# Performance work log

Hardware: AMD Instinct MI355X
Metric: run time of the kernel (lower is better)

Reference implementation:

```python
import jax, jax.numpy as jnp
import numpy as np

EPS = 1e-7  # K.epsilon()


def setup_inputs() -> dict:
    key = jax.random.key(0)
    k1, k2, k3, k4, k5, k6 = jax.random.split(key, 6)
    B, S, D = 128, 1024, 256
    ATT, QDIM = 128, 128
    inp = {
        "key": jax.random.normal(k1, (B, S, D), dtype=jnp.float32),
        "query": jax.random.normal(k2, (QDIM, 1), dtype=jnp.float32),
        "mask": jax.random.randint(k3, (B, S), 0, 2, dtype=jnp.int32),
        # learned params (keras 'normal' init ~ N(0, 0.05))
        "W": 0.05 * jax.random.normal(k4, (D, ATT), dtype=jnp.float32),
        "b": 0.05 * jax.random.normal(k5, (ATT,), dtype=jnp.float32),
        "W_u": 0.05 * jax.random.normal(k6, (ATT, QDIM), dtype=jnp.float32),
    }
    return inp


def reference(key, query, mask, W, b, W_u):
    # uit = tanh(key @ W + b): (B,S,ATT)
    uit = jnp.tanh(jnp.einsum("bsd,da->bsa", key, W) + b)
    # u = W_u @ query: (ATT,1)
    u = W_u @ query
    # scores: (B,S)
    ait = jnp.einsum("bsa,a->bs", uit, u[:, 0])
    ait = jnp.exp(ait)
    ait = ait * mask.astype(jnp.float32)
    ait = ait / (jnp.sum(ait, axis=1, keepdims=True) + EPS)
    # weighted sum over sequence -> (B,D); value == key
    out = jnp.einsum("bs,bsd->bd", ait, key)
    return out
```

## Files before the change

### kernel.cpp

```cpp
#include <hip/hip_runtime.h>
#include <hip/hip_bf16.h>
#include <math.h>

#define EPS_F 1e-7f

constexpr int Bn = 128, Sn = 1024, Dn = 256, ATTn = 128, QDn = 128;
constexpr int Mn = Bn * Sn;
constexpr int BM = 128;
constexpr int NBLK = Mn / BM;
constexpr int NJ = ATTn / 16;

typedef short short8 __attribute__((ext_vector_type(8)));
typedef float f32x4  __attribute__((ext_vector_type(4)));

__device__ inline void split_bf(float f, ushort& hi, ushort& lo) {
    uint fb = __float_as_uint(f);
    hi = (ushort)(fb >> 16);
    float hf = __uint_as_float(fb & 0xffff0000u);
    float lf = f - hf;
    __hip_bfloat16 lb = __float2bfloat16(lf);
    __builtin_memcpy(&lo, &lb, 2);
}

__device__ inline float tanh_fast(float x) {
    float cx = fminf(9.0f, fmaxf(-9.0f, x));
    float e = __builtin_amdgcn_exp2f(cx * 2.8853900817779268f);
    return (e - 1.0f) * __builtin_amdgcn_rcpf(e + 1.0f);
}

__device__ inline void gload_lds16(const void* g, void* lds_base) {
    __builtin_amdgcn_global_load_lds(
        (const __attribute__((address_space(1))) unsigned int*)g,
        (__attribute__((address_space(3))) unsigned int*)lds_base, 16, 0, 0);
}

#define MFMA_BF16 __builtin_amdgcn_mfma_f32_16x16x32_bf16


__global__ __launch_bounds__(256) void k_prep(
    const float* __restrict__ Wu, const float* __restrict__ q,
    float* __restrict__ u,
    const float* __restrict__ W,
    ushort* __restrict__ Bhi, ushort* __restrict__ Blo)
{
    if (blockIdx.x == 0) {
        __shared__ float qs[QDn];
        int t = threadIdx.x;
        if (t < QDn) qs[t] = q[t];
        __syncthreads();
        if (t < ATTn) {
            float acc = 0.f;
            #pragma unroll 8
            for (int j = 0; j < QDn; ++j) acc += Wu[t * QDn + j] * qs[j];
            u[t] = acc;
        }
        return;
    }
    int gid  = (blockIdx.x - 1) * 256 + threadIdx.x;
    int lane = gid & 63;
    int j    = (gid >> 6) & 7;
    int ks   = gid >> 9;
    int col  = j * 16 + (lane & 15);
    int kb   = ks * 32 + (lane >> 4) * 8;
    #pragma unroll
    for (int i = 0; i < 8; ++i) {
        float f = W[(size_t)(kb + i) * ATTn + col];
        ushort h, l;
        split_bf(f, h, l);
        size_t idx = (size_t)gid * 8 + i;
        Bhi[idx] = h; Blo[idx] = l;
    }
}

__device__ __forceinline__ void stage_quarter(
    float4* dst, const ushort* __restrict__ Bhi,
    const ushort* __restrict__ Blo, int q, int t, int w)
{
    #pragma unroll
    for (int i = 0; i < 4; ++i) {
        int c   = i * 512 + t;
        int ks2 = c >> 10;
        int hp  = (c >> 9) & 1;
        int idx = c & 511;
        const ushort* src = (hp ? Blo : Bhi)
                          + ((size_t)((q * 2 + ks2) * 512 + idx)) * 8;
        gload_lds16(src, dst + (i * 512 + w * 64));
    }
}

template<int KS>
__device__ __forceinline__ void kstep(
    float4* smem, const float* kb,
    float4 (&kv)[4][2], f32x4 (&acc)[NJ], int lane)
{
    const float4* buf = smem + ((KS >> 1) & 1) * 2048;
    constexpr int S  = KS & 3;
    constexpr int S2 = KS & 1;
    short8 ah, al;
    {
        float4 v0 = kv[S][0], v1 = kv[S][1];
        float f[8] = {v0.x, v0.y, v0.z, v0.w, v1.x, v1.y, v1.z, v1.w};
        #pragma unroll
        for (int i = 0; i < 8; ++i) {
            ushort h, l;
            split_bf(f[i], h, l);
            ah[i] = (short)h; al[i] = (short)l;
        }
    }
    if (KS + 4 < 8) {
        kv[S][0] = *(const float4*)(kb + (KS + 4) * 32);
        kv[S][1] = *(const float4*)(kb + (KS + 4) * 32 + 4);
    }
    const float4* Bh = buf + S2 * 1024 + lane;
    const float4* Bl = Bh + 512;
    short8 bh[3], bl[3];
    bh[0] = *(const short8*)(Bh);
    bl[0] = *(const short8*)(Bl);
    bh[1] = *(const short8*)(Bh + 64);
    bl[1] = *(const short8*)(Bl + 64);
    bh[2] = *(const short8*)(Bh + 128);
    bl[2] = *(const short8*)(Bl + 128);
    #pragma unroll
    for (int j = 0; j < NJ; ++j) {
        const int slot = j % 3;
        short8 cbh = bh[slot], cbl = bl[slot];
        if (j + 3 < NJ) {
            bh[slot] = *(const short8*)(Bh + (j + 3) * 64);
            bl[slot] = *(const short8*)(Bl + (j + 3) * 64);
        }
        acc[j] = MFMA_BF16(ah, cbh, acc[j], 0, 0, 0);
        acc[j] = MFMA_BF16(ah, cbl, acc[j], 0, 0, 0);
        acc[j] = MFMA_BF16(al, cbh, acc[j], 0, 0, 0);
    }
}

__global__ __launch_bounds__(512)
__attribute__((amdgpu_waves_per_eu(4, 4))) void k_scores(
    const float*  __restrict__ key,
    const ushort* __restrict__ Bhi, const ushort* __restrict__ Blo,
    const float*  __restrict__ bias, const float* __restrict__ u,
    const int*    __restrict__ mask,
    float* __restrict__ P, float* __restrict__ den)
{
    __shared__ float4 smem[4096];
    float*  esp   = (float*)smem;
    float4* partp = smem + 64;

    const int t    = threadIdx.x;
    const int lane = t & 63;
    const int w    = t >> 6;
    const int gb   = blockIdx.x;
    const int row0 = gb * BM;
    const int l15  = lane & 15;
    const int lg   = lane >> 4;

    const float* kb = key + (size_t)(row0 + w * 16 + l15) * Dn + lg * 8;

    f32x4 acc[NJ];
    #pragma unroll
    for (int j = 0; j < NJ; ++j) acc[j] = (f32x4){0.f, 0.f, 0.f, 0.f};

    float4 kv[4][2];
    #pragma unroll
    for (int s = 0; s < 4; ++s) {
        kv[s][0] = *(const float4*)(kb + s * 32);
        kv[s][1] = *(const float4*)(kb + s * 32 + 4);
    }

    stage_quarter(smem, Bhi, Blo, 0, t, w);
    __syncthreads();

    stage_quarter(smem + 2048, Bhi, Blo, 1, t, w);
    kstep<0>(smem, kb, kv, acc, lane);
    kstep<1>(smem, kb, kv, acc, lane);
    __syncthreads();

    stage_quarter(smem, Bhi, Blo, 2, t, w);
    kstep<2>(smem, kb, kv, acc, lane);
    kstep<3>(smem, kb, kv, acc, lane);
    __syncthreads();

    stage_quarter(smem + 2048, Bhi, Blo, 3, t, w);
    kstep<4>(smem, kb, kv, acc, lane);
    kstep<5>(smem, kb, kv, acc, lane);
    __syncthreads();

    kstep<6>(smem, kb, kv, acc, lane);
    kstep<7>(smem, kb, kv, acc, lane);
    __syncthreads();

    float s4[4] = {0.f, 0.f, 0.f, 0.f};
    #pragma unroll
    for (int j = 0; j < NJ; ++j) {
        int col = j * 16 + l15;
        float bv = bias[col], uvv = u[col];
        #pragma unroll
        for (int reg = 0; reg < 4; ++reg)
            s4[reg] += tanh_fast(acc[j][reg] + bv) * uvv;
    }
    #pragma unroll
    for (int reg = 0; reg < 4; ++reg) {
        float s = s4[reg];
        s += __shfl_xor(s, 1);
        s += __shfl_xor(s, 2);
        s += __shfl_xor(s, 4);
        s += __shfl_xor(s, 8);
        if (l15 == 0) {
            int rl = w * 16 + lg * 4 + reg;
            esp[rl] = __builtin_amdgcn_exp2f(s * 1.4426950408889634f)
                      * (float)mask[row0 + rl];
        }
    }
    __syncthreads();

    if (t < 64) {
        float v = esp[t] + esp[t + 64];
        #pragma unroll
        for (int m = 1; m < 64; m <<= 1) v += __shfl_xor(v, m);
        if (t == 0) den[gb] = v;
    }

    {
        const float4* kt = (const float4*)(key + (size_t)(row0 + w * 16) * Dn);
        float4 a2 = make_float4(0.f, 0.f, 0.f, 0.f);
        #pragma unroll 4
        for (int s2 = 0; s2 < 16; ++s2) {
            float wv   = esp[w * 16 + s2];
            float4 kvv = kt[(size_t)s2 * 64 + lane];
            a2.x += wv * kvv.x; a2.y += wv * kvv.y;
            a2.z += wv * kvv.z; a2.w += wv * kvv.w;
        }
        partp[w * 64 + lane] = a2;
    }
    __syncthreads();

    if (t < 64) {
        float4 o = partp[t];
        #pragma unroll
        for (int wv = 1; wv < 8; ++wv) {
            float4 p = partp[wv * 64 + t];
            o.x += p.x; o.y += p.y; o.z += p.z; o.w += p.w;
        }
        *(float4*)(P + (size_t)gb * Dn + t * 4) = o;
    }
}

__global__ __launch_bounds__(256) void k_final(const float* __restrict__ P,
        const float* __restrict__ den, float* __restrict__ out) {
    int b = blockIdx.x, t = threadIdx.x;
    float dtot = 0.f;
    #pragma unroll
    for (int k = 0; k < 8; ++k) dtot += den[b * 8 + k];
    float o = 0.f;
    #pragma unroll
    for (int k = 0; k < 8; ++k) o += P[(size_t)(b * 8 + k) * Dn + t];
    out[(size_t)b * Dn + t] = o / (dtot + EPS_F);
}

extern "C" void kernel_launch(void* const* d_in, const int* in_sizes, int n_in,
                              void* d_out, int out_size, void* d_ws, size_t ws_size,
                              hipStream_t stream) {
    const float* key   = (const float*)d_in[0];
    const float* query = (const float*)d_in[1];
    const int*   mask  = (const int*)d_in[2];
    const float* W     = (const float*)d_in[3];
    const float* bias  = (const float*)d_in[4];
    const float* Wu    = (const float*)d_in[5];
    float* out = (float*)d_out;

    char* ws = (char*)d_ws;
    float*  u   = (float*)(ws);
    ushort* Bhi = (ushort*)(ws + 512);
    ushort* Blo = (ushort*)(ws + 66048);
    float*  Pp  = (float*)(ws + 131584);
    float*  den = (float*)(ws + 1180160);

    hipLaunchKernelGGL(k_prep,   dim3(17),   dim3(256), 0, stream, Wu, query, u, W, Bhi, Blo);
    hipLaunchKernelGGL(k_scores, dim3(NBLK), dim3(512), 0, stream,
                       key, Bhi, Blo, bias, u, mask, Pp, den);
    hipLaunchKernelGGL(k_final,  dim3(Bn),   dim3(256), 0, stream, Pp, den, out);
}
```

Measured before the change: 57.88 us.

## Drop W low-bf16 split, stage whole W in LDS once, raise MFMA priority

Weights are now rounded to a single bf16 instead of a hi/lo pair, so each k-step needs two MFMAs instead of three and half the LDS traffic for B. Because the single-precision W now fits in 64 KB of LDS, it is loaded in one pass before the loop, which removes the double-buffered quarter staging and its intermediate barriers. It also wraps the MFMA loop in s_setprio and swaps waves_per_eu for launch_bounds min blocks. The cost is lower accuracy in the tanh pre-activation, since the low part of W is discarded.

```diff
diff --git a/kernel.cpp b/kernel.cpp
--- a/kernel.cpp
+++ b/kernel.cpp
@@ -41,7 +41,7 @@
     const float* __restrict__ Wu, const float* __restrict__ q,
     float* __restrict__ u,
     const float* __restrict__ W,
-    ushort* __restrict__ Bhi, ushort* __restrict__ Blo)
+    ushort* __restrict__ Bhi)
 {
     if (blockIdx.x == 0) {
         __shared__ float qs[QDn];
@@ -65,37 +65,18 @@
     #pragma unroll
     for (int i = 0; i < 8; ++i) {
         float f = W[(size_t)(kb + i) * ATTn + col];
-        ushort h, l;
-        split_bf(f, h, l);
-        size_t idx = (size_t)gid * 8 + i;
-        Bhi[idx] = h; Blo[idx] = l;
-    }
-}
-
-__device__ __forceinline__ void stage_quarter(
-    float4* dst, const ushort* __restrict__ Bhi,
-    const ushort* __restrict__ Blo, int q, int t, int w)
-{
-    #pragma unroll
-    for (int i = 0; i < 4; ++i) {
-        int c   = i * 512 + t;
-        int ks2 = c >> 10;
-        int hp  = (c >> 9) & 1;
-        int idx = c & 511;
-        const ushort* src = (hp ? Blo : Bhi)
-                          + ((size_t)((q * 2 + ks2) * 512 + idx)) * 8;
-        gload_lds16(src, dst + (i * 512 + w * 64));
+        __hip_bfloat16 h = __float2bfloat16(f);
+        ushort hu; __builtin_memcpy(&hu, &h, 2);
+        Bhi[(size_t)gid * 8 + i] = hu;
     }
 }
 
 template<int KS>
 __device__ __forceinline__ void kstep(
-    float4* smem, const float* kb,
+    const float4* smem, const float* kb,
     float4 (&kv)[4][2], f32x4 (&acc)[NJ], int lane)
 {
-    const float4* buf = smem + ((KS >> 1) & 1) * 2048;
-    constexpr int S  = KS & 3;
-    constexpr int S2 = KS & 1;
+    constexpr int S = KS & 3;
     short8 ah, al;
     {
         float4 v0 = kv[S][0], v1 = kv[S][1];
@@ -111,33 +92,27 @@
         kv[S][0] = *(const float4*)(kb + (KS + 4) * 32);
         kv[S][1] = *(const float4*)(kb + (KS + 4) * 32 + 4);
     }
-    const float4* Bh = buf + S2 * 1024 + lane;
-    const float4* Bl = Bh + 512;
-    short8 bh[3], bl[3];
+    const float4* Bh = smem + KS * 512 + lane;
+    short8 bh[3];
     bh[0] = *(const short8*)(Bh);
-    bl[0] = *(const short8*)(Bl);
     bh[1] = *(const short8*)(Bh + 64);
-    bl[1] = *(const short8*)(Bl + 64);
     bh[2] = *(const short8*)(Bh + 128);
-    bl[2] = *(const short8*)(Bl + 128);
+    __builtin_amdgcn_s_setprio(1);
     #pragma unroll
     for (int j = 0; j < NJ; ++j) {
         const int slot = j % 3;
-        short8 cbh = bh[slot], cbl = bl[slot];
-        if (j + 3 < NJ) {
+        short8 cbh = bh[slot];
+        if (j + 3 < NJ)
             bh[slot] = *(const short8*)(Bh + (j + 3) * 64);
-            bl[slot] = *(const short8*)(Bl + (j + 3) * 64);
-        }
         acc[j] = MFMA_BF16(ah, cbh, acc[j], 0, 0, 0);
-        acc[j] = MFMA_BF16(ah, cbl, acc[j], 0, 0, 0);
         acc[j] = MFMA_BF16(al, cbh, acc[j], 0, 0, 0);
     }
-}
-
-__global__ __launch_bounds__(512)
-__attribute__((amdgpu_waves_per_eu(4, 4))) void k_scores(
+    __builtin_amdgcn_s_setprio(0);
+}
+
+__global__ __launch_bounds__(512, 4) void k_scores(
     const float*  __restrict__ key,
-    const ushort* __restrict__ Bhi, const ushort* __restrict__ Blo,
+    const ushort* __restrict__ Bhi,
     const float*  __restrict__ bias, const float* __restrict__ u,
     const int*    __restrict__ mask,
     float* __restrict__ P, float* __restrict__ den)
@@ -167,24 +142,17 @@
         kv[s][1] = *(const float4*)(kb + s * 32 + 4);
     }
 
-    stage_quarter(smem, Bhi, Blo, 0, t, w);
-    __syncthreads();
-
-    stage_quarter(smem + 2048, Bhi, Blo, 1, t, w);
+    #pragma unroll
+    for (int i = 0; i < 8; ++i)
+        gload_lds16(Bhi + (size_t)(i * 512 + t) * 8, smem + (i * 512 + w * 64));
+    __syncthreads();
+
     kstep<0>(smem, kb, kv, acc, lane);
     kstep<1>(smem, kb, kv, acc, lane);
-    __syncthreads();
-
-    stage_quarter(smem, Bhi, Blo, 2, t, w);
     kstep<2>(smem, kb, kv, acc, lane);
     kstep<3>(smem, kb, kv, acc, lane);
-    __syncthreads();
-
-    stage_quarter(smem + 2048, Bhi, Blo, 3, t, w);
     kstep<4>(smem, kb, kv, acc, lane);
     kstep<5>(smem, kb, kv, acc, lane);
-    __syncthreads();
-
     kstep<6>(smem, kb, kv, acc, lane);
     kstep<7>(smem, kb, kv, acc, lane);
     __syncthreads();
@@ -271,12 +239,11 @@
     char* ws = (char*)d_ws;
     float*  u   = (float*)(ws);
     ushort* Bhi = (ushort*)(ws + 512);
-    ushort* Blo = (ushort*)(ws + 66048);
-    float*  Pp  = (float*)(ws + 131584);
-    float*  den = (float*)(ws + 1180160);
-
-    hipLaunchKernelGGL(k_prep,   dim3(17),   dim3(256), 0, stream, Wu, query, u, W, Bhi, Blo);
+    float*  Pp  = (float*)(ws + 66048);
+    float*  den = (float*)(ws + 1114624);
+
+    hipLaunchKernelGGL(k_prep,   dim3(17),   dim3(256), 0, stream, Wu, query, u, W, Bhi);
     hipLaunchKernelGGL(k_scores, dim3(NBLK), dim3(512), 0, stream,
-                       key, Bhi, Blo, bias, u, mask, Pp, den);
+                       key, Bhi, bias, u, mask, Pp, den);
     hipLaunchKernelGGL(k_final,  dim3(Bn),   dim3(256), 0, stream, Pp, den, out);
 }
```

Result: faster. 53.55 us (-7.5%).
